# Kernel tuning notes

Measured on AMD Instinct MI355X. Metric: run time of the kernel, lower is better.

Reference implementation:

```python
import jax, jax.numpy as jnp
import numpy as np

N_STATE = 256   # complex state size n (real state is 2n)
N_IN = 128
BATCH = 16
T_STEPS = 2048
H_STEP = 0.01
EPS = 1e-3
LAM_RE_MIN, LAM_RE_MAX, MAX_PHASE = -5.0, -0.5, 6.283


def setup_inputs() -> dict:
    rng = np.random.default_rng(0)
    n, nu = N_STATE, N_IN
    # trainable params (as in torch __init__)
    u1 = rng.random(n)
    u2 = rng.random(n) * 2.0 - 1.0
    alpha = np.log(-(u1 * (LAM_RE_MAX - LAM_RE_MIN) + LAM_RE_MIN)).astype(np.float32)
    theta = (MAX_PHASE * u2).astype(np.float32)
    B_re = (rng.standard_normal((n, nu)) / np.sqrt(2.0 * nu)).astype(np.float32)
    B_im = (rng.standard_normal((n, nu)) / np.sqrt(2.0 * nu)).astype(np.float32)
    # fixed basis-change buffers: rho (normalized), T_inv, P = rho @ T_inv, Pinv
    H1 = rng.standard_normal((n, n))
    H2 = rng.standard_normal((n, n))
    rho = np.block([[H1, -H2], [H2, H1]])
    rho = rho / np.linalg.norm(rho)
    I = np.eye(n)
    T_inv = (1.0 / np.sqrt(2.0)) * np.block([[I, I], [-1j * I, 1j * I]])
    P = rho.astype(np.complex128) @ T_inv
    Pinv = np.linalg.inv(P)
    key = jax.random.key(0)
    k1, k2 = jax.random.split(key)
    return {
        "xi_init": jax.random.normal(k1, (BATCH, 1, 2 * n), dtype=jnp.float32),
        "u_log": jax.random.normal(k2, (BATCH, T_STEPS, nu), dtype=jnp.float32),
        "alpha": jnp.asarray(alpha),
        "theta": jnp.asarray(theta),
        "B_re": jnp.asarray(B_re),
        "B_im": jnp.asarray(B_im),
        "P_re": jnp.asarray(P.real, dtype=jnp.float32),
        "P_im": jnp.asarray(P.imag, dtype=jnp.float32),
        "Pinv_re": jnp.asarray(Pinv.real, dtype=jnp.float32),
        "Pinv_im": jnp.asarray(Pinv.imag, dtype=jnp.float32),
        "T": T_STEPS,
    }


def reference(xi_init, u_log, alpha, theta, B_re, B_im, P_re, P_im, Pinv_re, Pinv_im, T):
    n = alpha.shape[0]
    lam = (-jnp.exp(alpha) - EPS) + 1j * theta          # (n,) complex64
    Bc = B_re + 1j * B_im                               # (n, nu)
    P = P_re + 1j * P_im                                # (2n, 2n)
    Pinv = Pinv_re + 1j * Pinv_im                       # (2n, 2n)
    xi0 = xi_init[:, 0, :]                              # (B, 2n) real

    def step(xi, u_t):
        # xi: (B, 2n) real state; u_t: (B, nu)
        x_tilde = xi.astype(jnp.complex64) @ Pinv.T     # (B, 2n) complex
        x_bar = x_tilde[:, :n]                          # (B, n)
        x_bar_dot = lam * x_bar + u_t.astype(jnp.complex64) @ Bc.T
        x_tilde_dot = jnp.concatenate([x_bar_dot, jnp.conj(x_bar_dot)], axis=-1)
        x_dot = (x_tilde_dot @ P.T).real                # (B, 2n)
        xi_new = xi + H_STEP * x_dot
        return xi_new, xi_new

    u_seq = jnp.swapaxes(u_log, 0, 1)                   # (T, B, nu)
    _, xs = jax.lax.scan(step, xi0, u_seq)              # (T, B, 2n)
    # torch _sim logs xi_init, then skips xi after t=0, logs xi after t=1..T-1
    x_log = jnp.concatenate([xi0[None], xs[1:]], axis=0)  # (T, B, 2n)
    return jnp.swapaxes(x_log, 0, 1)                    # (B, T, 2n)
```

## Files before the change

kernel.cpp:

```cpp
#include <hip/hip_runtime.h>
#include <hip/hip_bf16.h>
#include <cstddef>
#include <cstdint>

#define N_ST 256
#define TWO_N 512
#define NU 128
#define BATCH 16
#define TSTEPS 2048
#define MTOT (BATCH * TSTEPS)
#define H_STEP 0.01f
#define EPS_V 0.001f
#define NCHUNK 32
#define CHUNKL 64

typedef __attribute__((ext_vector_type(4))) float f32x4;
typedef __attribute__((ext_vector_type(4))) short s16x4;
typedef __attribute__((ext_vector_type(8))) short s16x8;

#define OFF_FPK    0
#define OFF_ZPK    8388608
#define OFF_UPK    16777216
#define OFF_WT     18874368
#define OFF_WF     19005440
#define OFF_D      19038208
#define OFF_XBAR0  19039232
#define OFF_E      19047424

static __device__ __forceinline__ float bf2f(short s) {
    return __uint_as_float(((unsigned)(unsigned short)s) << 16);
}

__global__ __launch_bounds__(256) void prep_all(
    const float* __restrict__ P_re, const float* __restrict__ P_im,
    const float* __restrict__ B_re, const float* __restrict__ B_im,
    const float* __restrict__ alpha, const float* __restrict__ theta,
    short* __restrict__ Wtpk, short* __restrict__ Wfpk,
    float* __restrict__ dbuf)
{
    int blk = blockIdx.x, tid = threadIdx.x;
    if (blk < 1024) {
        int idx = blk * 256 + tid;
        int j = idx >> 9, c = idx & 511;
        float v;
        if (c < N_ST) v = P_re[j * TWO_N + c] + P_re[j * TWO_N + c + N_ST];
        else          v = P_im[j * TWO_N + c] - P_im[j * TWO_N + c - N_ST];
        __hip_bfloat16 b = __float2bfloat16(v);
        Wtpk[((size_t)(j >> 4) * TWO_N + c) * 16 + (j & 15)] = *(short*)&b;
    } else if (blk < 1280) {
        int idx = (blk - 1024) * 256 + tid;
        int k = idx >> 9, c = idx & 511;
        float v = (c < N_ST) ? B_re[c * NU + k] : B_im[(c - N_ST) * NU + k];
        __hip_bfloat16 b = __float2bfloat16(H_STEP * v);
        Wfpk[((size_t)(c >> 4) * NU + k) * 16 + (c & 15)] = *(short*)&b;
    } else {
        int i = tid;
        float dr = 1.0f + H_STEP * (-expf(alpha[i]) - EPS_V);
        float di = H_STEP * theta[i];
        float pr = 1.0f, pi = 0.0f;
        for (int k = 0; k < CHUNKL; ++k) { float nr = pr * dr - pi * di; pi = pr * di + pi * dr; pr = nr; }
        dbuf[i] = dr; dbuf[N_ST + i] = di; dbuf[2 * N_ST + i] = pr; dbuf[3 * N_ST + i] = pi;
    }
}

__global__ __launch_bounds__(256) void xbar0_kernel(
    const float* __restrict__ Pinv_re, const float* __restrict__ Pinv_im,
    const float* __restrict__ xi0, float* __restrict__ xbar0)
{
    __shared__ float xs[BATCH * TWO_N];
    int tid = threadIdx.x;
#pragma unroll
    for (int q = 0; q < 8; ++q)
        *reinterpret_cast<float4*>(&xs[(q * 256 + tid) * 4]) =
            *reinterpret_cast<const float4*>(&xi0[(q * 256 + tid) * 4]);
    __syncthreads();

    int wv = tid >> 6, l = tid & 63;
    int i = blockIdx.x * 4 + wv;
    float rp[BATCH] = {}, ip[BATCH] = {};
#pragma unroll
    for (int q = 0; q < 8; ++q) {
        int j = q * 64 + l;
        float pr = Pinv_re[(size_t)i * TWO_N + j];
        float pi = Pinv_im[(size_t)i * TWO_N + j];
#pragma unroll
        for (int b = 0; b < BATCH; ++b) {
            float x = xs[b * TWO_N + j];
            rp[b] = fmaf(pr, x, rp[b]);
            ip[b] = fmaf(pi, x, ip[b]);
        }
    }
#pragma unroll
    for (int m = 1; m < 64; m <<= 1) {
#pragma unroll
        for (int b = 0; b < BATCH; ++b) {
            rp[b] += __shfl_xor(rp[b], m, 64);
            ip[b] += __shfl_xor(ip[b], m, 64);
        }
    }
    if (l == 0) {
#pragma unroll
        for (int b = 0; b < BATCH; ++b) {
            xbar0[b * TWO_N + i] = rp[b];
            xbar0[b * TWO_N + N_ST + i] = ip[b];
        }
    }
}

__global__ __launch_bounds__(256) void upack(const float* __restrict__ u, short* __restrict__ upk) {
    __shared__ short st[64 * 132];
    int tid = threadIdx.x, bid = blockIdx.x;
    const float* up = u + (size_t)bid * 8192;
#pragma unroll
    for (int q = 0; q < 8; ++q) {
        int idx = q * 1024 + tid * 4;
        float4 v = *reinterpret_cast<const float4*>(up + idx);
        int m = idx >> 7, k = idx & 127;
        s16x4 pv;
        __hip_bfloat16 b0 = __float2bfloat16(v.x); pv[0] = *(short*)&b0;
        __hip_bfloat16 b1 = __float2bfloat16(v.y); pv[1] = *(short*)&b1;
        __hip_bfloat16 b2 = __float2bfloat16(v.z); pv[2] = *(short*)&b2;
        __hip_bfloat16 b3 = __float2bfloat16(v.w); pv[3] = *(short*)&b3;
        *reinterpret_cast<__shared__ s16x4*>(&st[m * 132 + k]) = pv;
    }
    __syncthreads();
    short* op = upk + (size_t)bid * 8192;
#pragma unroll
    for (int q2 = 0; q2 < 4; ++q2) {
        int o = q2 * 2048 + tid * 8;
        int ml = o & 15, k = (o >> 4) & 127, sl = o >> 11;
        s16x8 w;
#pragma unroll
        for (int r = 0; r < 8; ++r) w[r] = st[(sl * 16 + ml + r) * 132 + k];
        *reinterpret_cast<s16x8*>(op + o) = w;
    }
}

template <int K, bool PACKOUT>
__global__ __launch_bounds__(256, 3) void gemm_mfma(const short* __restrict__ Apk,
                                                    const short* __restrict__ Bpk,
                                                    float* __restrict__ Cf,
                                                    short* __restrict__ Cp,
                                                    const float* __restrict__ xi0) {
    __shared__ __align__(1024) short lds[24576];
    const int tid = threadIdx.x;
    const int wid = tid >> 6, lane = tid & 63;
    const int m0 = blockIdx.x * 128, n0 = blockIdx.y * 128;
    const int wm = wid >> 1, wn = wid & 1;
    f32x4 acc[4][4] = {};
    const size_t slabStride = (size_t)K * 16;
    const unsigned ldsBase = (unsigned)(uintptr_t)(__attribute__((address_space(3))) short*)&lds[0];
    constexpr int NT = K / 32;

#define STAGE(buf, kk)                                                                              \
    do {                                                                                            \
        const short* gA0 = Apk + ((size_t)(m0 >> 4) + wid)     * slabStride + (size_t)(kk) * 16 + lane * 8; \
        const short* gA1 = Apk + ((size_t)(m0 >> 4) + wid + 4) * slabStride + (size_t)(kk) * 16 + lane * 8; \
        const short* gB0 = Bpk + ((size_t)(n0 >> 4) + wid)     * slabStride + (size_t)(kk) * 16 + lane * 8; \
        const short* gB1 = Bpk + ((size_t)(n0 >> 4) + wid + 4) * slabStride + (size_t)(kk) * 16 + lane * 8; \
        __builtin_amdgcn_global_load_lds((const __attribute__((address_space(1))) void*)gA0,        \
            (__attribute__((address_space(3))) void*)&lds[(buf) * 4096 + wid * 512], 16, 0, 0);     \
        __builtin_amdgcn_global_load_lds((const __attribute__((address_space(1))) void*)gA1,        \
            (__attribute__((address_space(3))) void*)&lds[(buf) * 4096 + (wid + 4) * 512], 16, 0, 0); \
        __builtin_amdgcn_global_load_lds((const __attribute__((address_space(1))) void*)gB0,        \
            (__attribute__((address_space(3))) void*)&lds[12288 + (buf) * 4096 + wid * 512], 16, 0, 0); \
        __builtin_amdgcn_global_load_lds((const __attribute__((address_space(1))) void*)gB1,        \
            (__attribute__((address_space(3))) void*)&lds[12288 + (buf) * 4096 + (wid + 4) * 512], 16, 0, 0); \
    } while (0)

    STAGE(0, 0);
    STAGE(1, 32);

#pragma unroll
    for (int t = 0; t < NT; ++t) {
        const int cur = t % 3;
        if (t + 2 < NT) STAGE((t + 2) % 3, (t + 2) * 32);

        if (t + 2 < NT)      asm volatile("s_waitcnt vmcnt(8)" ::: "memory");
        else if (t + 1 < NT) asm volatile("s_waitcnt vmcnt(4)" ::: "memory");
        else                 asm volatile("s_waitcnt vmcnt(0)" ::: "memory");
        __builtin_amdgcn_sched_barrier(0);
        __builtin_amdgcn_s_barrier();
        __builtin_amdgcn_sched_barrier(0);

        s16x4 al[4], ah[4], bl[4], bh[4];
        const unsigned aB = ldsBase + (unsigned)cur * 8192;
        const unsigned bB = ldsBase + 24576u + (unsigned)cur * 8192;
#pragma unroll
        for (int q = 0; q < 4; ++q) {
            unsigned ad = aB + ((unsigned)(wm * 4 + q) << 10) + ((unsigned)lane << 3);
            unsigned bd = bB + ((unsigned)(wn * 4 + q) << 10) + ((unsigned)lane << 3);
            asm volatile("ds_read_b64_tr_b16 %0, %1 offset:0"   : "=v"(al[q]) : "v"(ad));
            asm volatile("ds_read_b64_tr_b16 %0, %1 offset:512" : "=v"(ah[q]) : "v"(ad));
            asm volatile("ds_read_b64_tr_b16 %0, %1 offset:0"   : "=v"(bl[q]) : "v"(bd));
            asm volatile("ds_read_b64_tr_b16 %0, %1 offset:512" : "=v"(bh[q]) : "v"(bd));
        }
        asm volatile("s_waitcnt lgkmcnt(0)" ::: "memory");
        __builtin_amdgcn_sched_barrier(0);
        __builtin_amdgcn_s_barrier();
        __builtin_amdgcn_sched_barrier(0);

#pragma unroll
        for (int i = 0; i < 4; ++i) {
            s16x8 av = __builtin_shufflevector(al[i], ah[i], 0, 1, 2, 3, 4, 5, 6, 7);
#pragma unroll
            for (int j = 0; j < 4; ++j) {
                s16x8 bv = __builtin_shufflevector(bl[j], bh[j], 0, 1, 2, 3, 4, 5, 6, 7);
                acc[i][j] = __builtin_amdgcn_mfma_f32_16x16x32_bf16(av, bv, acc[i][j], 0, 0, 0);
            }
        }
    }
#undef STAGE

    const int cn = lane & 15;
    const int g4 = (lane >> 4) * 4;
    if (!PACKOUT) {
#pragma unroll
        for (int i = 0; i < 4; ++i) {
            int mrow = m0 + (wm * 4 + i) * 16 + g4;
#pragma unroll
            for (int j = 0; j < 4; ++j) {
                int ncol = n0 + (wn * 4 + j) * 16 + cn;
                float* cp = Cf + (size_t)mrow * TWO_N + ncol;
#pragma unroll
                for (int r = 0; r < 4; ++r) {
                    float v = acc[i][j][r];
                    if (((mrow + r) & (TSTEPS - 1)) == 0)
                        v = xi0[((mrow + r) >> 11) * TWO_N + ncol];
                    cp[(size_t)r * TWO_N] = v;
                }
            }
        }
    } else {
        __syncthreads();
#pragma unroll
        for (int i = 0; i < 4; ++i) {
            int s = wm * 4 + i;
#pragma unroll
            for (int j = 0; j < 4; ++j) {
                int cwt = wn * 64 + j * 16 + cn;
                s16x4 pv;
#pragma unroll
                for (int r = 0; r < 4; ++r) {
                    __hip_bfloat16 bb = __float2bfloat16(acc[i][j][r]);
                    pv[r] = *reinterpret_cast<short*>(&bb);
                }
                *reinterpret_cast<__shared__ s16x4*>(&lds[((s * 128 + cwt) << 4) + g4]) = pv;
            }
        }
        __syncthreads();
        size_t baseG = (size_t)(m0 >> 4) * ((size_t)TWO_N * 16) + (size_t)n0 * 16;
#pragma unroll
        for (int q = 0; q < 8; ++q) {
            *reinterpret_cast<s16x8*>(Cp + baseG + (size_t)q * (TWO_N * 16) + tid * 8) =
                *reinterpret_cast<const __shared__ s16x8*>(&lds[q * 2048 + tid * 8]);
        }
    }
}

__global__ __launch_bounds__(256) void scan_passA(const short* __restrict__ Fpk,
                                                  const float* __restrict__ dbuf,
                                                  float* __restrict__ e) {
    int b = blockIdx.x, c = blockIdx.y, i = threadIdx.x;
    float dr = dbuf[i], di = dbuf[N_ST + i];
    float re = 0.f, im = 0.f;
    int slab0 = (b * TSTEPS + c * CHUNKL) >> 4;
#pragma unroll
    for (int g = 0; g < 4; ++g) {
        const short* base = Fpk + (size_t)(slab0 + g) * 8192 + i * 16;
        s16x8 r0 = *reinterpret_cast<const s16x8*>(base);
        s16x8 r1 = *reinterpret_cast<const s16x8*>(base + 8);
        s16x8 i0 = *reinterpret_cast<const s16x8*>(base + 4096);
        s16x8 i1 = *reinterpret_cast<const s16x8*>(base + 4096 + 8);
#pragma unroll
        for (int j = 0; j < 16; ++j) {
            float fr = bf2f(j < 8 ? r0[j & 7] : r1[j & 7]);
            float fi = bf2f(j < 8 ? i0[j & 7] : i1[j & 7]);
            float nre = fmaf(dr, re, fmaf(-di, im, fr));
            float nim = fmaf(dr, im, fmaf(di, re, fi));
            re = nre; im = nim;
        }
    }
    size_t o = ((size_t)(b * NCHUNK + c)) * TWO_N;
    e[o + i] = re;
    e[o + N_ST + i] = im;
}

__global__ __launch_bounds__(256) void scan_passC(const short* __restrict__ Fpk,
                                                  const float* __restrict__ dbuf,
                                                  const float* __restrict__ e,
                                                  const float* __restrict__ xbar0,
                                                  short* __restrict__ Zpk) {
    int b = blockIdx.x, c = blockIdx.y, i = threadIdx.x;
    float dr = dbuf[i], di = dbuf[N_ST + i];
    float dLr = dbuf[2 * N_ST + i], dLi = dbuf[3 * N_ST + i];
    float re = xbar0[b * TWO_N + i], im = xbar0[b * TWO_N + N_ST + i];
    for (int cc = 0; cc < c; ++cc) {
        size_t o = ((size_t)(b * NCHUNK + cc)) * TWO_N;
        float er = e[o + i], ei = e[o + N_ST + i];
        float nre = fmaf(dLr, re, fmaf(-dLi, im, er));
        float nim = fmaf(dLr, im, fmaf(dLi, re, ei));
        re = nre; im = nim;
    }
    int slab0 = (b * TSTEPS + c * CHUNKL) >> 4;
#pragma unroll
    for (int g = 0; g < 4; ++g) {
        const short* base = Fpk + (size_t)(slab0 + g) * 8192 + i * 16;
        s16x8 r0 = *reinterpret_cast<const s16x8*>(base);
        s16x8 r1 = *reinterpret_cast<const s16x8*>(base + 8);
        s16x8 i0 = *reinterpret_cast<const s16x8*>(base + 4096);
        s16x8 i1 = *reinterpret_cast<const s16x8*>(base + 4096 + 8);
        s16x8 zr0, zr1, zi0, zi1;
#pragma unroll
        for (int j = 0; j < 16; ++j) {
            float fr = bf2f(j < 8 ? r0[j & 7] : r1[j & 7]);
            float fi = bf2f(j < 8 ? i0[j & 7] : i1[j & 7]);
            float nre = fmaf(dr, re, fmaf(-di, im, fr));
            float nim = fmaf(dr, im, fmaf(di, re, fi));
            re = nre; im = nim;
            __hip_bfloat16 br = __float2bfloat16(re), bi = __float2bfloat16(im);
            if (j < 8) { zr0[j & 7] = *(short*)&br; zi0[j & 7] = *(short*)&bi; }
            else       { zr1[j & 7] = *(short*)&br; zi1[j & 7] = *(short*)&bi; }
        }
        short* zb = Zpk + (size_t)(slab0 + g) * 8192 + i * 16;
        *reinterpret_cast<s16x8*>(zb)            = zr0;
        *reinterpret_cast<s16x8*>(zb + 8)        = zr1;
        *reinterpret_cast<s16x8*>(zb + 4096)     = zi0;
        *reinterpret_cast<s16x8*>(zb + 4096 + 8) = zi1;
    }
}

extern "C" void kernel_launch(void* const* d_in, const int* in_sizes, int n_in,
                              void* d_out, int out_size, void* d_ws, size_t ws_size,
                              hipStream_t stream) {
    const float* xi_init = (const float*)d_in[0];
    const float* u_log   = (const float*)d_in[1];
    const float* alpha   = (const float*)d_in[2];
    const float* theta   = (const float*)d_in[3];
    const float* B_re    = (const float*)d_in[4];
    const float* B_im    = (const float*)d_in[5];
    const float* P_re    = (const float*)d_in[6];
    const float* P_im    = (const float*)d_in[7];
    const float* Pinv_re = (const float*)d_in[8];
    const float* Pinv_im = (const float*)d_in[9];
    float* out = (float*)d_out;
    float* ws  = (float*)d_ws;

    short* Fpk  = (short*)(ws + OFF_FPK);
    short* Zpk  = (short*)(ws + OFF_ZPK);
    short* upk  = (short*)(ws + OFF_UPK);
    short* Wtpk = (short*)(ws + OFF_WT);
    short* Wfpk = (short*)(ws + OFF_WF);
    float* dbuf  = ws + OFF_D;
    float* xbar0 = ws + OFF_XBAR0;
    float* e     = ws + OFF_E;

    prep_all<<<1281, 256, 0, stream>>>(P_re, P_im, B_re, B_im, alpha, theta,
                                       Wtpk, Wfpk, dbuf);
    xbar0_kernel<<<64, 256, 0, stream>>>(Pinv_re, Pinv_im, xi_init, xbar0);
    upack<<<MTOT / 64, 256, 0, stream>>>(u_log, upk);

    gemm_mfma<NU, true><<<dim3(MTOT / 128, 4), 256, 0, stream>>>(
        upk, Wfpk, nullptr, Fpk, nullptr);

    scan_passA<<<dim3(BATCH, NCHUNK), 256, 0, stream>>>(Fpk, dbuf, e);
    scan_passC<<<dim3(BATCH, NCHUNK), 256, 0, stream>>>(Fpk, dbuf, e, xbar0, Zpk);

    gemm_mfma<TWO_N, false><<<dim3(MTOT / 128, 4), 256, 0, stream>>>(
        Zpk, Wtpk, out, nullptr, xi_init);
}
```

Before: 82.99 us.

## Enlarge GEMM tiles to 256x256 with 8 waves, double buffering and grouped block order

The MFMA GEMM moves from 128x128 tiles with 4 waves to 256x256 tiles with 8 waves per block. Each wave now computes a 128x64 sub-tile. Blocks are launched on a 1D grid with swizzled m/n indices so neighbouring blocks share A rows. The LDS pipeline goes from triple to double buffering, MFMA sections are wrapped in s_setprio, and the packed-output epilogue writes straight to global memory instead of staging through LDS. The goal is more operand reuse per loaded byte and better L2 locality. The costs are more accumulator registers, only 256 blocks for the whole GPU, and shallower prefetch.

```diff
diff --git a/kernel.cpp b/kernel.cpp
--- a/kernel.cpp
+++ b/kernel.cpp
@@ -137,17 +137,20 @@
 }
 
 template <int K, bool PACKOUT>
-__global__ __launch_bounds__(256, 3) void gemm_mfma(const short* __restrict__ Apk,
+__global__ __launch_bounds__(512, 4) void gemm_mfma(const short* __restrict__ Apk,
                                                     const short* __restrict__ Bpk,
                                                     float* __restrict__ Cf,
                                                     short* __restrict__ Cp,
                                                     const float* __restrict__ xi0) {
-    __shared__ __align__(1024) short lds[24576];
+    __shared__ __align__(1024) short lds[32768];
     const int tid = threadIdx.x;
     const int wid = tid >> 6, lane = tid & 63;
-    const int m0 = blockIdx.x * 128, n0 = blockIdx.y * 128;
-    const int wm = wid >> 1, wn = wid & 1;
-    f32x4 acc[4][4] = {};
+    const int l = blockIdx.x;
+    const int mb = ((l >> 4) << 3) | (l & 7);
+    const int nb = (l >> 3) & 1;
+    const int m0 = mb * 256, n0 = nb * 256;
+    const int wm = wid >> 2, wn = wid & 3;
+    f32x4 acc[8][4] = {};
     const size_t slabStride = (size_t)K * 16;
     const unsigned ldsBase = (unsigned)(uintptr_t)(__attribute__((address_space(3))) short*)&lds[0];
     constexpr int NT = K / 32;
@@ -155,53 +158,55 @@
 #define STAGE(buf, kk)                                                                              \
     do {                                                                                            \
         const short* gA0 = Apk + ((size_t)(m0 >> 4) + wid)     * slabStride + (size_t)(kk) * 16 + lane * 8; \
-        const short* gA1 = Apk + ((size_t)(m0 >> 4) + wid + 4) * slabStride + (size_t)(kk) * 16 + lane * 8; \
+        const short* gA1 = Apk + ((size_t)(m0 >> 4) + wid + 8) * slabStride + (size_t)(kk) * 16 + lane * 8; \
         const short* gB0 = Bpk + ((size_t)(n0 >> 4) + wid)     * slabStride + (size_t)(kk) * 16 + lane * 8; \
-        const short* gB1 = Bpk + ((size_t)(n0 >> 4) + wid + 4) * slabStride + (size_t)(kk) * 16 + lane * 8; \
+        const short* gB1 = Bpk + ((size_t)(n0 >> 4) + wid + 8) * slabStride + (size_t)(kk) * 16 + lane * 8; \
         __builtin_amdgcn_global_load_lds((const __attribute__((address_space(1))) void*)gA0,        \
-            (__attribute__((address_space(3))) void*)&lds[(buf) * 4096 + wid * 512], 16, 0, 0);     \
+            (__attribute__((address_space(3))) void*)&lds[(buf) * 8192 + wid * 512], 16, 0, 0);     \
         __builtin_amdgcn_global_load_lds((const __attribute__((address_space(1))) void*)gA1,        \
-            (__attribute__((address_space(3))) void*)&lds[(buf) * 4096 + (wid + 4) * 512], 16, 0, 0); \
+            (__attribute__((address_space(3))) void*)&lds[(buf) * 8192 + (wid + 8) * 512], 16, 0, 0); \
         __builtin_amdgcn_global_load_lds((const __attribute__((address_space(1))) void*)gB0,        \
-            (__attribute__((address_space(3))) void*)&lds[12288 + (buf) * 4096 + wid * 512], 16, 0, 0); \
+            (__attribute__((address_space(3))) void*)&lds[16384 + (buf) * 8192 + wid * 512], 16, 0, 0); \
         __builtin_amdgcn_global_load_lds((const __attribute__((address_space(1))) void*)gB1,        \
-            (__attribute__((address_space(3))) void*)&lds[12288 + (buf) * 4096 + (wid + 4) * 512], 16, 0, 0); \
+            (__attribute__((address_space(3))) void*)&lds[16384 + (buf) * 8192 + (wid + 8) * 512], 16, 0, 0); \
     } while (0)
 
     STAGE(0, 0);
-    STAGE(1, 32);
 
 #pragma unroll
     for (int t = 0; t < NT; ++t) {
-        const int cur = t % 3;
-        if (t + 2 < NT) STAGE((t + 2) % 3, (t + 2) * 32);
-
-        if (t + 2 < NT)      asm volatile("s_waitcnt vmcnt(8)" ::: "memory");
-        else if (t + 1 < NT) asm volatile("s_waitcnt vmcnt(4)" ::: "memory");
-        else                 asm volatile("s_waitcnt vmcnt(0)" ::: "memory");
+        const int cur = t & 1;
+        if (t + 1 < NT) STAGE(cur ^ 1, (t + 1) * 32);
+
+        if (t + 1 < NT) asm volatile("s_waitcnt vmcnt(4)" ::: "memory");
+        else            asm volatile("s_waitcnt vmcnt(0)" ::: "memory");
         __builtin_amdgcn_sched_barrier(0);
         __builtin_amdgcn_s_barrier();
         __builtin_amdgcn_sched_barrier(0);
 
-        s16x4 al[4], ah[4], bl[4], bh[4];
-        const unsigned aB = ldsBase + (unsigned)cur * 8192;
-        const unsigned bB = ldsBase + 24576u + (unsigned)cur * 8192;
-#pragma unroll
-        for (int q = 0; q < 4; ++q) {
-            unsigned ad = aB + ((unsigned)(wm * 4 + q) << 10) + ((unsigned)lane << 3);
-            unsigned bd = bB + ((unsigned)(wn * 4 + q) << 10) + ((unsigned)lane << 3);
-            asm volatile("ds_read_b64_tr_b16 %0, %1 offset:0"   : "=v"(al[q]) : "v"(ad));
-            asm volatile("ds_read_b64_tr_b16 %0, %1 offset:512" : "=v"(ah[q]) : "v"(ad));
-            asm volatile("ds_read_b64_tr_b16 %0, %1 offset:0"   : "=v"(bl[q]) : "v"(bd));
-            asm volatile("ds_read_b64_tr_b16 %0, %1 offset:512" : "=v"(bh[q]) : "v"(bd));
+        s16x4 al[8], ah[8], bl[4], bh[4];
+        const unsigned aB = ldsBase + (unsigned)cur * 16384u;
+        const unsigned bB = ldsBase + 32768u + (unsigned)cur * 16384u;
+#pragma unroll
+        for (int i = 0; i < 8; ++i) {
+            unsigned ad = aB + ((unsigned)(wm * 8 + i) << 10) + ((unsigned)lane << 3);
+            asm volatile("ds_read_b64_tr_b16 %0, %1 offset:0"   : "=v"(al[i]) : "v"(ad));
+            asm volatile("ds_read_b64_tr_b16 %0, %1 offset:512" : "=v"(ah[i]) : "v"(ad));
+        }
+#pragma unroll
+        for (int j = 0; j < 4; ++j) {
+            unsigned bd = bB + ((unsigned)(wn * 4 + j) << 10) + ((unsigned)lane << 3);
+            asm volatile("ds_read_b64_tr_b16 %0, %1 offset:0"   : "=v"(bl[j]) : "v"(bd));
+            asm volatile("ds_read_b64_tr_b16 %0, %1 offset:512" : "=v"(bh[j]) : "v"(bd));
         }
         asm volatile("s_waitcnt lgkmcnt(0)" ::: "memory");
         __builtin_amdgcn_sched_barrier(0);
         __builtin_amdgcn_s_barrier();
         __builtin_amdgcn_sched_barrier(0);
 
-#pragma unroll
-        for (int i = 0; i < 4; ++i) {
+        __builtin_amdgcn_s_setprio(1);
+#pragma unroll
+        for (int i = 0; i < 8; ++i) {
             s16x8 av = __builtin_shufflevector(al[i], ah[i], 0, 1, 2, 3, 4, 5, 6, 7);
 #pragma unroll
             for (int j = 0; j < 4; ++j) {
@@ -209,6 +214,7 @@
                 acc[i][j] = __builtin_amdgcn_mfma_f32_16x16x32_bf16(av, bv, acc[i][j], 0, 0, 0);
             }
         }
+        __builtin_amdgcn_s_setprio(0);
     }
 #undef STAGE
 
@@ -216,11 +222,11 @@
     const int g4 = (lane >> 4) * 4;
     if (!PACKOUT) {
 #pragma unroll
-        for (int i = 0; i < 4; ++i) {
-            int mrow = m0 + (wm * 4 + i) * 16 + g4;
+        for (int i = 0; i < 8; ++i) {
+            int mrow = m0 + wm * 128 + i * 16 + g4;
 #pragma unroll
             for (int j = 0; j < 4; ++j) {
-                int ncol = n0 + (wn * 4 + j) * 16 + cn;
+                int ncol = n0 + wn * 64 + j * 16 + cn;
                 float* cp = Cf + (size_t)mrow * TWO_N + ncol;
 #pragma unroll
                 for (int r = 0; r < 4; ++r) {
@@ -232,28 +238,20 @@
             }
         }
     } else {
-        __syncthreads();
-#pragma unroll
-        for (int i = 0; i < 4; ++i) {
-            int s = wm * 4 + i;
+#pragma unroll
+        for (int i = 0; i < 8; ++i) {
+            size_t slab = (size_t)((m0 >> 4) + wm * 8 + i);
 #pragma unroll
             for (int j = 0; j < 4; ++j) {
-                int cwt = wn * 64 + j * 16 + cn;
+                int n = n0 + wn * 64 + j * 16 + cn;
                 s16x4 pv;
 #pragma unroll
                 for (int r = 0; r < 4; ++r) {
                     __hip_bfloat16 bb = __float2bfloat16(acc[i][j][r]);
                     pv[r] = *reinterpret_cast<short*>(&bb);
                 }
-                *reinterpret_cast<__shared__ s16x4*>(&lds[((s * 128 + cwt) << 4) + g4]) = pv;
+                *reinterpret_cast<s16x4*>(Cp + slab * 8192 + (size_t)n * 16 + g4) = pv;
             }
-        }
-        __syncthreads();
-        size_t baseG = (size_t)(m0 >> 4) * ((size_t)TWO_N * 16) + (size_t)n0 * 16;
-#pragma unroll
-        for (int q = 0; q < 8; ++q) {
-            *reinterpret_cast<s16x8*>(Cp + baseG + (size_t)q * (TWO_N * 16) + tid * 8) =
-                *reinterpret_cast<const __shared__ s16x8*>(&lds[q * 2048 + tid * 8]);
         }
     }
 }
@@ -360,12 +358,12 @@
     xbar0_kernel<<<64, 256, 0, stream>>>(Pinv_re, Pinv_im, xi_init, xbar0);
     upack<<<MTOT / 64, 256, 0, stream>>>(u_log, upk);
 
-    gemm_mfma<NU, true><<<dim3(MTOT / 128, 4), 256, 0, stream>>>(
+    gemm_mfma<NU, true><<<256, 512, 0, stream>>>(
         upk, Wfpk, nullptr, Fpk, nullptr);
 
     scan_passA<<<dim3(BATCH, NCHUNK), 256, 0, stream>>>(Fpk, dbuf, e);
     scan_passC<<<dim3(BATCH, NCHUNK), 256, 0, stream>>>(Fpk, dbuf, e, xbar0, Zpk);
 
-    gemm_mfma<TWO_N, false><<<dim3(MTOT / 128, 4), 256, 0, stream>>>(
+    gemm_mfma<TWO_N, false><<<256, 512, 0, stream>>>(
         Zpk, Wtpk, out, nullptr, xi_init);
 }
```

New measurement: 299.8 us. 3.61x slower.
